# Kernel optimization log

Hardware: AMD Instinct MI355X
Metric: run time of the kernel (lower is better)

Reference implementation:

```python
import jax, jax.numpy as jnp
import numpy as np

N, IN, OUT, T = 65536, 256, 256, 8


def setup_inputs() -> dict:
    key = jax.random.key(0)
    k1, k2, k3, k4 = jax.random.split(key, 4)
    x = jax.random.normal(k1, (N, IN), dtype=jnp.float32)
    types = jax.random.randint(k2, (N,), 0, T, dtype=jnp.int32)
    # xavier_uniform for W: limit = sqrt(6 / (fan_in + fan_out)) with fan computed
    # on the last two dims (out_size, in_size)
    limit = float(np.sqrt(6.0 / (IN + OUT)))
    W = jax.random.uniform(k3, (T, OUT, IN), dtype=jnp.float32, minval=-limit, maxval=limit)
    # original inits b to zeros; use small random values so the bias path is exercised
    b = 0.01 * jax.random.normal(k4, (T, OUT), dtype=jnp.float32)
    return {"x": x, "types": types, "W": W, "b": b}


def reference(x, types, W, b):
    # out[i] = W[types[i]] @ x[i] + b[types[i]]
    # Grouped-GEMM expressed as a loop over the small fixed set of types,
    # avoiding the huge [N, OUT, IN] gather of W[types].
    num_types = W.shape[0]
    out = b[types]  # [N, OUT]
    for t in range(num_types):
        mask = (types == t)[:, None]  # [N, 1]
        out = out + jnp.where(mask, x @ W[t].T, jnp.float32(0.0))
    return out
```

## Files before the change

kernel.cpp:

```cpp
#include <hip/hip_runtime.h>
#include <hip/hip_bf16.h>
#include <stdint.h>


#define NROWS 65536
#define NTYPES 8
#define KDIM 256
#define ODIM 256
#define BM 128
#define BN 256
#define BK 64
#define HB 256
#define MAXTILES 640

typedef __attribute__((ext_vector_type(8))) short short8;
typedef __attribute__((ext_vector_type(4))) float f32x4;

__device__ __forceinline__ unsigned short f2bf(float f) {
    unsigned int u = __float_as_uint(f);
    u += 0x7fffu + ((u >> 16) & 1u);
    return (unsigned short)(u >> 16);
}

__global__ void hist_kernel(const int* __restrict__ types,
                            const float* __restrict__ W,
                            unsigned short* __restrict__ Wb,
                            int* __restrict__ blockHist) {
    __shared__ int h[NTYPES];
    const int tid = threadIdx.x;
    if (tid < NTYPES) h[tid] = 0;
    __syncthreads();
    const int i = blockIdx.x * 256 + tid;
    atomicAdd(&h[types[i]], 1);
    #pragma unroll
    for (int r = 0; r < 2; ++r) {
        int j = blockIdx.x * 512 + r * 256 + tid;
        float4 v = ((const float4*)W)[j];
        ushort4 p;
        p.x = f2bf(v.x); p.y = f2bf(v.y); p.z = f2bf(v.z); p.w = f2bf(v.w);
        ((ushort4*)Wb)[j] = p;
    }
    __syncthreads();
    if (tid < NTYPES) blockHist[blockIdx.x * NTYPES + tid] = h[tid];
}

__global__ void scan_kernel(const int* __restrict__ blockHist,
                            int* __restrict__ blockBase,
                            int* __restrict__ typeBase,
                            int4* __restrict__ tiles,
                            int* __restrict__ tileCount) {
    __shared__ int v[HB * NTYPES];
    __shared__ int scnt[NTYPES];
    __shared__ int sTypeBase[NTYPES], sTileBase[NTYPES + 1];
    const int tid = threadIdx.x;
    for (int j = tid; j < HB * NTYPES; j += 256) v[j] = blockHist[j];
    __syncthreads();

    const int t = tid >> 5;
    const int l = tid & 31;
    int s[8];
    int sum = 0;
    #pragma unroll
    for (int m = 0; m < 8; ++m) {
        s[m] = sum;
        sum += v[(l * 8 + m) * NTYPES + t];
    }
    int incl = sum;
    #pragma unroll
    for (int d = 1; d < 32; d <<= 1) {
        int y = __shfl_up(incl, d, 32);
        if (l >= d) incl += y;
    }
    const int excl = incl - sum;
    #pragma unroll
    for (int m = 0; m < 8; ++m)
        blockBase[(l * 8 + m) * NTYPES + t] = excl + s[m];
    if (l == 31) scnt[t] = incl;
    __syncthreads();

    if (tid == 0) {
        int rowacc = 0, tileacc = 0;
        for (int q = 0; q < NTYPES; ++q) {
            sTypeBase[q] = rowacc; typeBase[q] = rowacc; rowacc += scnt[q];
            sTileBase[q] = tileacc; tileacc += (scnt[q] + BM - 1) / BM;
        }
        sTileBase[NTYPES] = tileacc;
        tileCount[0] = tileacc;
    }
    __syncthreads();
    const int tc = sTileBase[NTYPES];
    for (int j = tid; j < tc; j += 256) {
        int q = 0;
        while (q < NTYPES - 1 && j >= sTileBase[q + 1]) ++q;
        tiles[j] = make_int4(q, (j - sTileBase[q]) * BM, sTypeBase[q], scnt[q]);
    }
}

__global__ void scatter_kernel(const int* __restrict__ types,
                               const int* __restrict__ blockBase,
                               const int* __restrict__ typeBase,
                               int* __restrict__ idx) {
    __shared__ int h[NTYPES];
    __shared__ int base[NTYPES];
    const int tid = threadIdx.x;
    if (tid < NTYPES) {
        h[tid] = 0;
        base[tid] = typeBase[tid] + blockBase[blockIdx.x * NTYPES + tid];
    }
    __syncthreads();
    const int i = blockIdx.x * 256 + tid;
    const int t = types[i];
    int r = atomicAdd(&h[t], 1);
    idx[base[t] + r] = i;
}

__global__ __launch_bounds__(512, 4)
void gemm_kernel(const float* __restrict__ x,
                 const float* __restrict__ bias,
                 const unsigned short* __restrict__ Wb,
                 const int* __restrict__ tileCount,
                 const int4* __restrict__ tiles,
                 const int* __restrict__ idx,
                 float* __restrict__ out) {
    if ((int)blockIdx.x >= tileCount[0]) return;
    const int4 td = tiles[blockIdx.x];
    const int t = td.x, m0 = td.y, rbase = td.z, count = td.w;
    const int rem = count - m0;

    __shared__ unsigned short As[BM * BK];
    __shared__ unsigned short Bs[BN * BK];

    const int tid = threadIdx.x;
    const int wave = tid >> 6;
    const int lane = tid & 63;
    const int lr = lane & 15;
    const int lq = lane >> 4;
    const int wm = (wave & 1) * 64;
    const int wn = (wave >> 1) * 64;

    const int* rowIdx = idx + rbase + m0;

    const int srow = tid >> 4;
    const int sc = tid & 15;
    const float* aptr[4];
    #pragma unroll
    for (int j = 0; j < 4; ++j) {
        int m = j * 32 + srow;
        aptr[j] = x + (size_t)rowIdx[m < rem ? m : 0] * KDIM + sc * 4;
    }

    float breg[4];
    #pragma unroll
    for (int j = 0; j < 4; ++j) breg[j] = bias[t * ODIM + wn + j * 16 + lr];

    const int bschunk = (lane & 7) ^ (lane >> 3);
    const unsigned short* bsrc0 = Wb + (size_t)t * ODIM * KDIM + (size_t)bschunk * 8;

    f32x4 acc[4][4] = {};
    char* AsB = (char*)As;
    char* BsB = (char*)Bs;

    for (int k0 = 0; k0 < KDIM; k0 += BK) {
        #pragma unroll
        for (int it = 0; it < 4; ++it) {
            int dbyte = it * 8192 + wave * 1024;
            int row = (dbyte >> 7) + (lane >> 3);
            const unsigned short* src = bsrc0 + (size_t)row * KDIM + k0;
            __builtin_amdgcn_global_load_lds(
                (const __attribute__((address_space(1))) void*)src,
                (__attribute__((address_space(3))) void*)(BsB + dbyte),
                16, 0, 0);
        }
        #pragma unroll
        for (int j = 0; j < 4; ++j) {
            int row = j * 32 + srow;
            const float4 v = *(const float4*)(aptr[j] + k0);
            ushort4 p;
            p.x = f2bf(v.x); p.y = f2bf(v.y); p.z = f2bf(v.z); p.w = f2bf(v.w);
            int ch = (sc >> 1) ^ (row & 7);
            *(ushort4*)(AsB + row * 128 + ch * 16 + (sc & 1) * 8) = p;
        }
        __syncthreads();

        #pragma unroll
        for (int kh = 0; kh < 2; ++kh) {
            short8 af[4], bfr[4];
            #pragma unroll
            for (int q = 0; q < 4; ++q) {
                int arow = wm + q * 16 + lr;
                int ach = ((kh << 2) + lq) ^ (arow & 7);
                af[q] = *(const short8*)(AsB + arow * 128 + ach * 16);
            }
            #pragma unroll
            for (int q = 0; q < 4; ++q) {
                int brow = wn + q * 16 + lr;
                int bch = ((kh << 2) + lq) ^ (brow & 7);
                bfr[q] = *(const short8*)(BsB + brow * 128 + bch * 16);
            }
            #pragma unroll
            for (int q = 0; q < 4; ++q)
                #pragma unroll
                for (int j = 0; j < 4; ++j)
                    acc[q][j] = __builtin_amdgcn_mfma_f32_16x16x32_bf16(
                        af[q], bfr[j], acc[q][j], 0, 0, 0);
        }
        __syncthreads();
    }

    #pragma unroll
    for (int q = 0; q < 4; ++q) {
        #pragma unroll
        for (int r = 0; r < 4; ++r) {
            int lm = wm + q * 16 + lq * 4 + r;
            if (lm < rem) {
                size_t orow = (size_t)rowIdx[lm] * ODIM;
                #pragma unroll
                for (int j = 0; j < 4; ++j)
                    out[orow + wn + j * 16 + lr] = acc[q][j][r] + breg[j];
            }
        }
    }
}

extern "C" void kernel_launch(void* const* d_in, const int* in_sizes, int n_in,
                              void* d_out, int out_size, void* d_ws, size_t ws_size,
                              hipStream_t stream) {
    const float* x     = (const float*)d_in[0];
    const int*   types = (const int*)d_in[1];
    const float* W     = (const float*)d_in[2];
    const float* b     = (const float*)d_in[3];
    float* out = (float*)d_out;

    char* ws = (char*)d_ws;
    int*  tileCount = (int*)ws;
    int*  typeBase  = (int*)(ws + 128);
    int*  blockHist = (int*)(ws + 512);
    int*  blockBase = (int*)(ws + 9216);
    int4* tiles     = (int4*)(ws + 17408);
    int*  idx       = (int*)(ws + 32768);
    unsigned short* Wb = (unsigned short*)(ws + 294912);

    hist_kernel<<<HB, 256, 0, stream>>>(types, W, Wb, blockHist);
    scan_kernel<<<1, 256, 0, stream>>>(blockHist, blockBase, typeBase, tiles, tileCount);
    scatter_kernel<<<HB, 256, 0, stream>>>(types, blockBase, typeBase, idx);
    gemm_kernel<<<dim3(MAXTILES, 1), 512, 0, stream>>>(x, b, Wb, tileCount, tiles, idx, out);
}
```

Before: 143.9 us.

## Pre-permute x into type-sorted bf16 buffer and split GEMM over N

The scatter kernel now also converts x to bf16 and writes it into a contiguous, type-sorted buffer. The GEMM can then stream A tiles with direct global-to-LDS loads instead of gathered fp32 loads converted in registers. The GEMM tile shrinks to 128 columns with a second grid dimension over the output columns, and blocks drop to 256 threads. This costs an extra write and read of a 32 MB bf16 copy of x, and each A tile is now loaded twice, once per column half.

```diff
diff --git a/kernel.cpp b/kernel.cpp
--- a/kernel.cpp
+++ b/kernel.cpp
@@ -8,10 +8,10 @@
 #define KDIM 256
 #define ODIM 256
 #define BM 128
-#define BN 256
+#define BN 128
 #define BK 64
 #define HB 256
-#define MAXTILES 640
+#define MAXTILES 544
 
 typedef __attribute__((ext_vector_type(8))) short short8;
 typedef __attribute__((ext_vector_type(4))) float f32x4;
@@ -30,8 +30,7 @@
     const int tid = threadIdx.x;
     if (tid < NTYPES) h[tid] = 0;
     __syncthreads();
-    const int i = blockIdx.x * 256 + tid;
-    atomicAdd(&h[types[i]], 1);
+    atomicAdd(&h[types[blockIdx.x * 256 + tid]], 1);
     #pragma unroll
     for (int r = 0; r < 2; ++r) {
         int j = blockIdx.x * 512 + r * 256 + tid;
@@ -96,26 +95,43 @@
     }
 }
 
-__global__ void scatter_kernel(const int* __restrict__ types,
+__global__ void permute_kernel(const float* __restrict__ x,
+                               const int* __restrict__ types,
                                const int* __restrict__ blockBase,
                                const int* __restrict__ typeBase,
-                               int* __restrict__ idx) {
-    __shared__ int h[NTYPES];
-    __shared__ int base[NTYPES];
+                               int* __restrict__ idx,
+                               unsigned short* __restrict__ xs) {
+    __shared__ int h[NTYPES], base[NTYPES];
+    __shared__ int slot_s[256];
     const int tid = threadIdx.x;
     if (tid < NTYPES) {
         h[tid] = 0;
         base[tid] = typeBase[tid] + blockBase[blockIdx.x * NTYPES + tid];
     }
     __syncthreads();
-    const int i = blockIdx.x * 256 + tid;
-    const int t = types[i];
+    const int row = blockIdx.x * 256 + tid;
+    const int t = types[row];
     int r = atomicAdd(&h[t], 1);
-    idx[base[t] + r] = i;
-}
-
-__global__ __launch_bounds__(512, 4)
-void gemm_kernel(const float* __restrict__ x,
+    int slot = base[t] + r;
+    slot_s[tid] = slot;
+    idx[slot] = row;
+    __syncthreads();
+
+    const int g = tid >> 6;
+    const int l = tid & 63;
+    const size_t r0 = (size_t)blockIdx.x * 256;
+    #pragma unroll 4
+    for (int m = 0; m < 64; ++m) {
+        int i = g * 64 + m;
+        float4 v = *(const float4*)(x + (r0 + i) * KDIM + l * 4);
+        ushort4 p;
+        p.x = f2bf(v.x); p.y = f2bf(v.y); p.z = f2bf(v.z); p.w = f2bf(v.w);
+        *(ushort4*)(xs + (size_t)slot_s[i] * KDIM + l * 4) = p;
+    }
+}
+
+__global__ __launch_bounds__(256, 4)
+void gemm_kernel(const unsigned short* __restrict__ xs,
                  const float* __restrict__ bias,
                  const unsigned short* __restrict__ Wb,
                  const int* __restrict__ tileCount,
@@ -125,6 +141,7 @@
     if ((int)blockIdx.x >= tileCount[0]) return;
     const int4 td = tiles[blockIdx.x];
     const int t = td.x, m0 = td.y, rbase = td.z, count = td.w;
+    const int n0 = blockIdx.y * BN;
     const int rem = count - m0;
 
     __shared__ unsigned short As[BM * BK];
@@ -135,26 +152,16 @@
     const int lane = tid & 63;
     const int lr = lane & 15;
     const int lq = lane >> 4;
-    const int wm = (wave & 1) * 64;
-    const int wn = (wave >> 1) * 64;
-
-    const int* rowIdx = idx + rbase + m0;
-
-    const int srow = tid >> 4;
-    const int sc = tid & 15;
-    const float* aptr[4];
-    #pragma unroll
-    for (int j = 0; j < 4; ++j) {
-        int m = j * 32 + srow;
-        aptr[j] = x + (size_t)rowIdx[m < rem ? m : 0] * KDIM + sc * 4;
-    }
+    const int wm = (wave >> 1) * 64;
+    const int wn = (wave & 1) * 64;
+
+    const int schunk = (lane & 7) ^ ((lane >> 3) & 7);
+    const unsigned short* asrc0 = xs + (size_t)(rbase + m0) * KDIM + (size_t)schunk * 8;
+    const unsigned short* bsrc0 = Wb + ((size_t)t * ODIM + n0) * KDIM + (size_t)schunk * 8;
 
     float breg[4];
     #pragma unroll
-    for (int j = 0; j < 4; ++j) breg[j] = bias[t * ODIM + wn + j * 16 + lr];
-
-    const int bschunk = (lane & 7) ^ (lane >> 3);
-    const unsigned short* bsrc0 = Wb + (size_t)t * ODIM * KDIM + (size_t)bschunk * 8;
+    for (int j = 0; j < 4; ++j) breg[j] = bias[t * ODIM + n0 + wn + j * 16 + lr];
 
     f32x4 acc[4][4] = {};
     char* AsB = (char*)As;
@@ -162,23 +169,15 @@
 
     for (int k0 = 0; k0 < KDIM; k0 += BK) {
         #pragma unroll
-        for (int it = 0; it < 4; ++it) {
-            int dbyte = it * 8192 + wave * 1024;
-            int row = (dbyte >> 7) + (lane >> 3);
-            const unsigned short* src = bsrc0 + (size_t)row * KDIM + k0;
+        for (int issue = 0; issue < 4; ++issue) {
+            int dbyte = issue * 4096 + wave * 1024;
+            int row = issue * 32 + wave * 8 + (lane >> 3);
             __builtin_amdgcn_global_load_lds(
-                (const __attribute__((address_space(1))) void*)src,
-                (__attribute__((address_space(3))) void*)(BsB + dbyte),
-                16, 0, 0);
-        }
-        #pragma unroll
-        for (int j = 0; j < 4; ++j) {
-            int row = j * 32 + srow;
-            const float4 v = *(const float4*)(aptr[j] + k0);
-            ushort4 p;
-            p.x = f2bf(v.x); p.y = f2bf(v.y); p.z = f2bf(v.z); p.w = f2bf(v.w);
-            int ch = (sc >> 1) ^ (row & 7);
-            *(ushort4*)(AsB + row * 128 + ch * 16 + (sc & 1) * 8) = p;
+                (const __attribute__((address_space(1))) void*)(asrc0 + (size_t)row * KDIM + k0),
+                (__attribute__((address_space(3))) void*)(AsB + dbyte), 16, 0, 0);
+            __builtin_amdgcn_global_load_lds(
+                (const __attribute__((address_space(1))) void*)(bsrc0 + (size_t)row * KDIM + k0),
+                (__attribute__((address_space(3))) void*)(BsB + dbyte), 16, 0, 0);
         }
         __syncthreads();
 
@@ -207,6 +206,7 @@
         __syncthreads();
     }
 
+    const int* rowIdx = idx + rbase + m0;
     #pragma unroll
     for (int q = 0; q < 4; ++q) {
         #pragma unroll
@@ -216,7 +216,7 @@
                 size_t orow = (size_t)rowIdx[lm] * ODIM;
                 #pragma unroll
                 for (int j = 0; j < 4; ++j)
-                    out[orow + wn + j * 16 + lr] = acc[q][j][r] + breg[j];
+                    out[orow + n0 + wn + j * 16 + lr] = acc[q][j][r] + breg[j];
             }
         }
     }
@@ -235,13 +235,14 @@
     int*  tileCount = (int*)ws;
     int*  typeBase  = (int*)(ws + 128);
     int*  blockHist = (int*)(ws + 512);
-    int*  blockBase = (int*)(ws + 9216);
-    int4* tiles     = (int4*)(ws + 17408);
-    int*  idx       = (int*)(ws + 32768);
-    unsigned short* Wb = (unsigned short*)(ws + 294912);
+    int*  blockBase = (int*)(ws + 8704);
+    int4* tiles     = (int4*)(ws + 16896);
+    int*  idx       = (int*)(ws + 25600);
+    unsigned short* Wb = (unsigned short*)(ws + 287744);
+    unsigned short* xs = (unsigned short*)(ws + 1336320);
 
     hist_kernel<<<HB, 256, 0, stream>>>(types, W, Wb, blockHist);
     scan_kernel<<<1, 256, 0, stream>>>(blockHist, blockBase, typeBase, tiles, tileCount);
-    scatter_kernel<<<HB, 256, 0, stream>>>(types, blockBase, typeBase, idx);
-    gemm_kernel<<<dim3(MAXTILES, 1), 512, 0, stream>>>(x, b, Wb, tileCount, tiles, idx, out);
-}
+    permute_kernel<<<HB, 256, 0, stream>>>(x, types, blockBase, typeBase, idx, xs);
+    gemm_kernel<<<dim3(MAXTILES, 2), 256, 0, stream>>>(xs, b, Wb, tileCount, tiles, idx, out);
+}
```

New measurement: 157.5 us. +9.4%, slower.
